# Optimization experiments

Measured on AMD Instinct MI355X. Metric: run time of the kernel, lower is better.

The kernel has to match this reference:

```python
import jax, jax.numpy as jnp
import numpy as np

V, D_IN = 32000, 300      # vocab, embedding dim (GRU input_size=300)
N, T = 4096, 64           # total nodes across batched graphs, tokens per node
B, NPG = 64, 64           # graphs, nodes per graph
E = 65536                 # total edges (avg degree 16)
RH, GH = 256, 256         # rnn_hidden_dim, gnn_hidden_dim


def gru_cell(x_proj, h, W_hh, b_hh):
    # x_proj = x @ W_ih.T + b_ih, shape [N, 3H]; PyTorch GRU gate order (r, z, n)
    gh = h @ W_hh.T + b_hh
    xr, xz, xn = jnp.split(x_proj, 3, axis=-1)
    hr, hz, hn = jnp.split(gh, 3, axis=-1)
    r = jax.nn.sigmoid(xr + hr)
    z = jax.nn.sigmoid(xz + hz)
    n = jnp.tanh(xn + r * hn)
    return (1.0 - z) * n + z * h


def setup_inputs() -> dict:
    key = jax.random.key(0)
    ks = jax.random.split(key, 16)
    tokens = jax.random.randint(ks[0], (N, T), 0, V)
    # edges live within a single graph (dgl.batch keeps graphs disjoint)
    edge_graph = jnp.arange(E) // (E // B)
    edge_src = edge_graph * NPG + jax.random.randint(ks[1], (E,), 0, NPG)
    edge_dst = edge_graph * NPG + jax.random.randint(ks[2], (E,), 0, NPG)
    graph_id = jnp.arange(N) // NPG
    local = jnp.arange(N) % NPG
    # node types: 0=history, 1=last_sentence (one per graph), 2=response (one per graph)
    node_type = jnp.where(local == NPG - 2, 1, jnp.where(local == NPG - 1, 2, 0))
    s = 0.02
    p = lambda k, shape: jax.random.normal(k, shape, dtype=jnp.float32) * s
    return dict(
        tokens=tokens, edge_src=edge_src, edge_dst=edge_dst,
        graph_id=graph_id, node_type=node_type,
        emb_table=p(ks[3], (V, D_IN)),
        W_ih_f=p(ks[4], (3 * RH, D_IN)), W_hh_f=p(ks[5], (3 * RH, RH)),
        b_ih_f=jnp.zeros((3 * RH,), jnp.float32), b_hh_f=jnp.zeros((3 * RH,), jnp.float32),
        W_ih_b=p(ks[6], (3 * RH, D_IN)), W_hh_b=p(ks[7], (3 * RH, RH)),
        b_ih_b=jnp.zeros((3 * RH,), jnp.float32), b_hh_b=jnp.zeros((3 * RH,), jnp.float32),
        W_g1=p(ks[8], (2 * RH, GH)), b_g1=jnp.zeros((GH,), jnp.float32),
        W_g2=p(ks[9], (GH, GH)), b_g2=jnp.zeros((GH,), jnp.float32),
        W_g3=p(ks[10], (GH, GH)), b_g3=jnp.zeros((GH,), jnp.float32),
        W_g4=p(ks[11], (GH, GH)), b_g4=jnp.zeros((GH,), jnp.float32),
    )


def reference(tokens, edge_src, edge_dst, graph_id, node_type, emb_table,
              W_ih_f, W_hh_f, b_ih_f, b_hh_f,
              W_ih_b, W_hh_b, b_ih_b, b_hh_b,
              W_g1, b_g1, W_g2, b_g2, W_g3, b_g3, W_g4, b_g4):
    x = emb_table[tokens]  # [N, T, 300]
    # Module keeps only output[:, -1, :]:
    #   forward half  = final forward hidden state (full scan over T)
    #   backward half = backward state after processing only timestep T-1
    #                   (i.e. one GRU cell step from zero state) -- exact math.
    xp_f = jnp.einsum('ntd,gd->ntg', x, W_ih_f) + b_ih_f  # [N, T, 3H]
    h0 = jnp.zeros((N, RH), x.dtype)

    def step(h, xp_t):
        return gru_cell(xp_t, h, W_hh_f, b_hh_f), None

    h_fwd, _ = jax.lax.scan(step, h0, jnp.swapaxes(xp_f, 0, 1))
    xp_b = x[:, -1] @ W_ih_b.T + b_ih_b
    h_bwd = gru_cell(xp_b, h0, W_hh_b, b_hh_b)
    h = jnp.concatenate([h_fwd, h_bwd], axis=-1)  # [N, 2H]

    # 4 GCN layers: sum-aggregate neighbor features (copy_src -> sum), then linear + ReLU
    for W, b in ((W_g1, b_g1), (W_g2, b_g2), (W_g3, b_g3), (W_g4, b_g4)):
        agg = jax.ops.segment_sum(h[edge_src], edge_dst, num_segments=N)
        h = jax.nn.relu(agg @ W + b)

    # per-graph readout by node type
    hist_m = (node_type == 0).astype(h.dtype)[:, None]
    last_m = (node_type == 1).astype(h.dtype)[:, None]
    resp_m = (node_type == 2).astype(h.dtype)[:, None]
    hist_sum = jax.ops.segment_sum(h * hist_m, graph_id, num_segments=B)
    hist_cnt = jax.ops.segment_sum(hist_m, graph_id, num_segments=B)
    batched_hist = hist_sum / hist_cnt
    batched_last = jax.ops.segment_sum(h * last_m, graph_id, num_segments=B)
    batched_resp = jax.ops.segment_sum(h * resp_m, graph_id, num_segments=B)
    return (batched_hist, batched_last, batched_resp)
```

## Files before the change

### kernel.cpp

```cpp
#include <hip/hip_runtime.h>
#include <cstddef>

#define NN_ 4096
#define TT_ 64
#define DIN 300
#define DINP 320
#define RH_ 256
#define G3_ 768
#define BB_ 64
#define EE_ 65536

typedef short bf16x8 __attribute__((ext_vector_type(8)));
typedef float f32x4 __attribute__((ext_vector_type(4)));
typedef unsigned short u16;

__device__ __forceinline__ u16 f2bf(float f) {
    unsigned u = __builtin_bit_cast(unsigned, f);
    u += 0x7fff + ((u >> 16) & 1);
    return (u16)(u >> 16);
}
__device__ __forceinline__ float bf2f(u16 v) {
    return __builtin_bit_cast(float, (unsigned)v << 16);
}

__device__ __forceinline__ void gload16(const void* g, void* l) {
    __builtin_amdgcn_global_load_lds(
        (const __attribute__((address_space(1))) unsigned*)g,
        (__attribute__((address_space(3))) unsigned*)l, 16, 0, 0);
}

#define MFMA16 __builtin_amdgcn_mfma_f32_16x16x32_bf16

__global__ void k_zero(float* __restrict__ p, long n) {
    for (long i = (long)blockIdx.x * blockDim.x + threadIdx.x; i < n;
         i += (long)gridDim.x * blockDim.x)
        p[i] = 0.f;
}

__global__ void k_cvt(const float* __restrict__ src, u16* __restrict__ dst,
                      int R, int C, int Cp) {
    long total = (long)R * Cp;
    for (long i = (long)blockIdx.x * blockDim.x + threadIdx.x; i < total;
         i += (long)gridDim.x * blockDim.x) {
        int r = (int)(i / Cp);
        int c = (int)(i - (long)r * Cp);
        dst[i] = (c < C) ? f2bf(src[(size_t)r * C + c]) : (u16)0;
    }
}

__global__ void k_cvtT(const float* __restrict__ W, u16* __restrict__ Wt, int K) {
    int total = 256 * K;
    for (int i = blockIdx.x * blockDim.x + threadIdx.x; i < total;
         i += gridDim.x * blockDim.x) {
        int c = i / K, k = i - c * K;
        Wt[i] = f2bf(W[(size_t)k * 256 + c]);
    }
}

__global__ void k_buildA(const int* __restrict__ src, const int* __restrict__ dst,
                         float* __restrict__ A) {
    int e = blockIdx.x * blockDim.x + threadIdx.x;
    if (e < EE_) {
        int g = src[e] >> 6, i = dst[e] & 63, j = src[e] & 63;
        atomicAdd(&A[(((g << 6) + i) << 6) + j], 1.f);
    }
}

__global__ __launch_bounds__(256) void k_trans(const float* __restrict__ h, int C,
                                               u16* __restrict__ hT) {
    __shared__ u16 Ls[64][72];
    int r0 = blockIdx.x * 64, c0 = blockIdx.y * 64;
    int tid = threadIdx.x;
    int r = tid >> 2, cq = tid & 3;
#pragma unroll
    for (int i = 0; i < 4; i++) {
        float4 v = *(const float4*)(h + (size_t)(r0 + r) * C + c0 + cq * 16 + i * 4);
        Ls[r][cq * 16 + i * 4 + 0] = f2bf(v.x);
        Ls[r][cq * 16 + i * 4 + 1] = f2bf(v.y);
        Ls[r][cq * 16 + i * 4 + 2] = f2bf(v.z);
        Ls[r][cq * 16 + i * 4 + 3] = f2bf(v.w);
    }
    __syncthreads();
    int c = tid >> 2, rq = tid & 3;
    u16 tmp[16];
#pragma unroll
    for (int i = 0; i < 16; i++) tmp[i] = Ls[rq * 16 + i][c];
    u16* o = hT + (size_t)(c0 + c) * NN_ + r0 + rq * 16;
    *(uint4*)o = ((const uint4*)tmp)[0];
    *(uint4*)(o + 8) = ((const uint4*)tmp)[1];
}

__global__ __launch_bounds__(256) void k_xproj(
    const u16* __restrict__ embbf, const u16* __restrict__ Wx,
    const float* __restrict__ bih, const float* __restrict__ bhh,
    u16* __restrict__ XP)
{
    __shared__ __align__(16) u16 As[2][64 * 32];
    __shared__ __align__(16) u16 Bs[2][64 * 32];
    const int tid = threadIdx.x;
    const int v0 = blockIdx.x * 64, c0 = blockIdx.y * 64;
    const int sr = tid >> 2, sq = tid & 3;
    const u16* pa = embbf + (size_t)(v0 + sr) * DINP + sq * 8;
    const u16* pb = Wx + (size_t)(c0 + sr) * DINP + sq * 8;

    const int lane = tid & 63, wave = tid >> 6;
    const int wr = wave >> 1, wc = wave & 1;
    const int l15 = lane & 15, l4 = lane >> 4;
    const int aoff = (wr * 32 + l15) * 32 + l4 * 8;
    const int boff = (wc * 32 + l15) * 32 + l4 * 8;
    f32x4 acc[2][2] = {};

    gload16(pa, &As[0][tid * 8]);
    gload16(pb, &Bs[0][tid * 8]);
    __syncthreads();
    constexpr int NSK = DINP / 32;
#pragma unroll
    for (int s = 0; s < NSK; s++) {
        if (s + 1 < NSK) {
            gload16(pa + (s + 1) * 32, &As[(s + 1) & 1][tid * 8]);
            gload16(pb + (s + 1) * 32, &Bs[(s + 1) & 1][tid * 8]);
        }
        const int b = s & 1;
        bf16x8 a0 = *(const bf16x8*)&As[b][aoff];
        bf16x8 a1 = *(const bf16x8*)&As[b][aoff + 512];
        bf16x8 b0 = *(const bf16x8*)&Bs[b][boff];
        bf16x8 b1 = *(const bf16x8*)&Bs[b][boff + 512];
        acc[0][0] = MFMA16(a0, b0, acc[0][0], 0, 0, 0);
        acc[0][1] = MFMA16(a0, b1, acc[0][1], 0, 0, 0);
        acc[1][0] = MFMA16(a1, b0, acc[1][0], 0, 0, 0);
        acc[1][1] = MFMA16(a1, b1, acc[1][1], 0, 0, 0);
        __syncthreads();
    }
#pragma unroll
    for (int fj = 0; fj < 2; fj++) {
        const int c = c0 + wc * 32 + fj * 16 + l15;
        const float bb = bih[c] + (c < 512 ? bhh[c] : 0.f);
#pragma unroll
        for (int fi = 0; fi < 2; fi++)
#pragma unroll
            for (int rg = 0; rg < 4; rg++) {
                const int v = v0 + wr * 32 + fi * 16 + l4 * 4 + rg;
                XP[(size_t)v * G3_ + c] = f2bf(acc[fi][fj][rg] + bb);
            }
    }
}

__global__ __launch_bounds__(512, 2) void k_scan(
    const int* __restrict__ tokens,
    const u16* __restrict__ XPROJ,
    const u16* __restrict__ Wh,
    const float* __restrict__ bhh,
    float* __restrict__ HA)
{
    __shared__ __align__(16) u16 hS[16 * RH_];
    __shared__ __align__(16) u16 XPs[3 * 16 * 256];
    __shared__ int toks[16 * 68];

    const int tid = threadIdx.x;
    const int n0 = blockIdx.x * 16;
    const int lane = tid & 63, wave = tid >> 6;
    const int l15 = lane & 15, l4 = lane >> 4;
    const int c0w = wave * 32;

    for (int idx = tid; idx < 16 * TT_; idx += 512) {
        int row = idx >> 6, tt = idx & 63;
        toks[row * 68 + tt] = tokens[(n0 + row) * TT_ + tt];
    }
    ((unsigned long long*)hS)[tid] = 0ull;
    ((unsigned long long*)hS)[512 + tid] = 0ull;

    bf16x8 Bv[3][2][8];
#pragma unroll
    for (int g = 0; g < 3; ++g)
#pragma unroll
        for (int f = 0; f < 2; ++f)
#pragma unroll
            for (int ks = 0; ks < 8; ++ks) {
                Bv[g][f][ks] = *(const bf16x8*)(
                    Wh + (size_t)(g * 256 + c0w + f * 16 + l15) * RH_ + ks * 32 + l4 * 8);
                asm volatile("" : "+v"(Bv[g][f][ks]));
            }

    const float bhn0 = bhh[512 + c0w + l15];
    const float bhn1 = bhh[512 + c0w + 16 + l15];

    const int srow = tid >> 5, sch = tid & 31;
    const int ssw = (((sch * 16) ^ ((srow >> 2) << 5)) >> 1);

    auto STAGE_XP = [&](int t) {
        int tok = toks[srow * 68 + t];
        const u16* src = XPROJ + (size_t)tok * G3_ + ssw;
#pragma unroll
        for (int g = 0; g < 3; ++g)
            gload16(src + g * 256, XPs + g * 4096 + tid * 8);
    };

    __syncthreads();

    STAGE_XP(0);

    f32x4 hprev[2] = {};

#pragma unroll 1
    for (int t = 0; t < TT_; ++t) {
        f32x4 acc[3][2];
#pragma unroll
        for (int g = 0; g < 3; ++g) { acc[g][0] = f32x4{}; acc[g][1] = f32x4{}; }
#pragma unroll
        for (int ks = 0; ks < 8; ++ks) {
            const int aa = (l15 * 512 + ks * 64 + l4 * 16) ^ ((l15 & 7) << 4);
            bf16x8 a = *(const bf16x8*)((const char*)hS + aa);
#pragma unroll
            for (int g = 0; g < 3; ++g) {
                acc[g][0] = MFMA16(a, Bv[g][0][ks], acc[g][0], 0, 0, 0);
                acc[g][1] = MFMA16(a, Bv[g][1][ks], acc[g][1], 0, 0, 0);
            }
        }
        __syncthreads();

#pragma unroll
        for (int f = 0; f < 2; ++f) {
            const int cc = c0w + f * 16 + l15;
            const float bhn = f == 0 ? bhn0 : bhn1;
#pragma unroll
            for (int rg = 0; rg < 4; ++rg) {
                const int r = l4 * 4 + rg;
                const int xb = r * 256 + ((((cc * 2) ^ ((r >> 2) << 5))) >> 1);
                float xr = bf2f(XPs[xb]);
                float xz = bf2f(XPs[4096 + xb]);
                float xn = bf2f(XPs[8192 + xb]);
                float gr = acc[0][f][rg];
                float gz = acc[1][f][rg];
                float gn = acc[2][f][rg];
                float hp = hprev[f][rg];
                float rr = 1.f / (1.f + __expf(-(xr + gr)));
                float zz = 1.f / (1.f + __expf(-(xz + gz)));
                float pre = xn + rr * (gn + bhn);
                float nv = 2.f / (1.f + __expf(-2.f * pre)) - 1.f;
                float hnew = (1.f - zz) * nv + zz * hp;
                hprev[f][rg] = hnew;
                if (t < TT_ - 1) {
                    const int ba = (r * 512 + cc * 2) ^ ((r & 7) << 4);
                    *(u16*)((char*)hS + ba) = f2bf(hnew);
                } else {
                    HA[(size_t)(n0 + r) * 512 + cc] = hnew;
                }
            }
        }
        __syncthreads();
        if (t < TT_ - 1) STAGE_XP(t + 1);
    }
}

template<bool XONLY>
__global__ __launch_bounds__(256) void k_step(
    const int* __restrict__ tokens, int t,
    const u16* __restrict__ embbf, const u16* __restrict__ Wx,
    const u16* __restrict__ Wh,
    const float* __restrict__ bih, const float* __restrict__ bhh,
    const u16* __restrict__ hbf_in, const float* __restrict__ hf_in,
    float* __restrict__ outf, int ostride, u16* __restrict__ outbf)
{
    constexpr int NSX = DINP / 32;
    constexpr int NS  = XONLY ? NSX : NSX + RH_ / 32;

    __shared__ __align__(16) u16 As[2][32 * 32];
    __shared__ __align__(16) u16 Bs[2][3 * 64 * 32];

    const int tid = threadIdx.x;
    const int n0 = blockIdx.x * 32;
    const int c0 = blockIdx.y * 64;

    const int sr = tid >> 2;
    const int sq = tid & 3;
    const int tok = (tid < 128) ? tokens[(n0 + sr) * TT_ + t] : 0;
    const u16* ax  = embbf + (size_t)tok * DINP + sq * 8;
    const u16* ah  = XONLY ? ax : hbf_in + (size_t)(n0 + sr) * RH_ + sq * 8;
    const u16* bx0 = Wx + (size_t)(0 * 256 + c0 + sr) * DINP + sq * 8;
    const u16* bx1 = Wx + (size_t)(1 * 256 + c0 + sr) * DINP + sq * 8;
    const u16* bx2 = Wx + (size_t)(2 * 256 + c0 + sr) * DINP + sq * 8;
    const u16* bh0 = XONLY ? ax : Wh + (size_t)(0 * 256 + c0 + sr) * RH_ + sq * 8;
    const u16* bh1 = XONLY ? ax : Wh + (size_t)(1 * 256 + c0 + sr) * RH_ + sq * 8;
    const u16* bh2 = XONLY ? ax : Wh + (size_t)(2 * 256 + c0 + sr) * RH_ + sq * 8;

    auto STAGE = [&](int b, int s) {
        u16* db = &Bs[b][tid * 8];
        if (s < NSX) {
            int kk = s * 32;
            if (tid < 128) gload16(ax + kk, &As[b][tid * 8]);
            gload16(bx0 + kk, db);
            gload16(bx1 + kk, db + 2048);
            gload16(bx2 + kk, db + 4096);
        } else {
            int kk = (s - NSX) * 32;
            if (tid < 128) gload16(ah + kk, &As[b][tid * 8]);
            gload16(bh0 + kk, db);
            gload16(bh1 + kk, db + 2048);
            gload16(bh2 + kk, db + 4096);
        }
    };

    const int lane = tid & 63;
    const int wave = tid >> 6;
    const int wr = wave >> 1, wc = wave & 1;
    const int l15 = lane & 15, l4 = lane >> 4;

    f32x4 aR[2] = {}, aZ[2] = {}, aXN[2] = {}, aHN[2] = {};

    const int aoff = (wr * 16 + l15) * 32 + l4 * 8;
    const int boff = (wc * 32 + l15) * 32 + l4 * 8;

    auto COMPUTE = [&](int b, bool xp) {
        bf16x8 a0 = *(const bf16x8*)&As[b][aoff];
        const u16* B = &Bs[b][0];
        bf16x8 r0 = *(const bf16x8*)&B[boff];
        bf16x8 r1 = *(const bf16x8*)&B[boff + 512];
        bf16x8 z0 = *(const bf16x8*)&B[2048 + boff];
        bf16x8 z1 = *(const bf16x8*)&B[2048 + boff + 512];
        bf16x8 n0f = *(const bf16x8*)&B[4096 + boff];
        bf16x8 n1f = *(const bf16x8*)&B[4096 + boff + 512];
        aR[0] = MFMA16(a0, r0, aR[0], 0, 0, 0);
        aR[1] = MFMA16(a0, r1, aR[1], 0, 0, 0);
        aZ[0] = MFMA16(a0, z0, aZ[0], 0, 0, 0);
        aZ[1] = MFMA16(a0, z1, aZ[1], 0, 0, 0);
        if (xp) {
            aXN[0] = MFMA16(a0, n0f, aXN[0], 0, 0, 0);
            aXN[1] = MFMA16(a0, n1f, aXN[1], 0, 0, 0);
        } else {
            aHN[0] = MFMA16(a0, n0f, aHN[0], 0, 0, 0);
            aHN[1] = MFMA16(a0, n1f, aHN[1], 0, 0, 0);
        }
    };

    STAGE(0, 0);
    __syncthreads();
#pragma unroll
    for (int s = 0; s < NS; ++s) {
        if (s + 1 < NS) STAGE((s + 1) & 1, s + 1);
        COMPUTE(s & 1, s < NSX);
        __syncthreads();
    }

#pragma unroll
    for (int fj = 0; fj < 2; ++fj) {
        const int c = c0 + wc * 32 + fj * 16 + l15;
        const float bR  = bih[c] + bhh[c];
        const float bZ  = bih[256 + c] + bhh[256 + c];
        const float bXN = bih[512 + c];
        const float bHN = bhh[512 + c];
#pragma unroll
        for (int rg = 0; rg < 4; ++rg) {
            const int n = n0 + wr * 16 + l4 * 4 + rg;
            float r  = 1.f / (1.f + __expf(-(aR[fj][rg] + bR)));
            float z  = 1.f / (1.f + __expf(-(aZ[fj][rg] + bZ)));
            float pre = aXN[fj][rg] + bXN + r * (aHN[fj][rg] + bHN);
            float nv = 2.f / (1.f + __expf(-2.f * pre)) - 1.f;
            float hp = XONLY ? 0.f : hf_in[(size_t)n * RH_ + c];
            float h  = (1.f - z) * nv + z * hp;
            outf[(size_t)n * ostride + c] = h;
            if (!XONLY) outbf[(size_t)n * RH_ + c] = f2bf(h);
        }
    }
}

__global__ __launch_bounds__(256) void k_agg(
    const u16* __restrict__ Abf, const u16* __restrict__ hT,
    u16* __restrict__ aggbf, int C)
{
    const int g = blockIdx.x, ct = blockIdx.y;
    const int lane = threadIdx.x & 63, wave = threadIdx.x >> 6;
    const int wi = wave >> 1, wcC = wave & 1;
    const int l15 = lane & 15, l4 = lane >> 4;
    f32x4 acc[2][2] = {};
#pragma unroll
    for (int kc = 0; kc < 2; kc++) {
        bf16x8 af[2], bf_[2];
#pragma unroll
        for (int fi = 0; fi < 2; fi++)
            af[fi] = *(const bf16x8*)(Abf + ((size_t)g * 64 + wi * 32 + fi * 16 + l15) * 64
                                      + kc * 32 + l4 * 8);
#pragma unroll
        for (int fj = 0; fj < 2; fj++)
            bf_[fj] = *(const bf16x8*)(hT + (size_t)(ct * 64 + wcC * 32 + fj * 16 + l15) * NN_
                                       + g * 64 + kc * 32 + l4 * 8);
#pragma unroll
        for (int fi = 0; fi < 2; fi++)
#pragma unroll
            for (int fj = 0; fj < 2; fj++)
                acc[fi][fj] = MFMA16(af[fi], bf_[fj], acc[fi][fj], 0, 0, 0);
    }
#pragma unroll
    for (int fi = 0; fi < 2; fi++)
#pragma unroll
        for (int fj = 0; fj < 2; fj++)
#pragma unroll
            for (int rg = 0; rg < 4; rg++) {
                int n = g * 64 + wi * 32 + fi * 16 + l4 * 4 + rg;
                int c = ct * 64 + wcC * 32 + fj * 16 + l15;
                aggbf[(size_t)n * C + c] = f2bf(acc[fi][fj][rg]);
            }
}

template<int K>
__global__ __launch_bounds__(256) void k_gcnM(
    const u16* __restrict__ Ag, const u16* __restrict__ Wt,
    const float* __restrict__ bias, float* __restrict__ outF)
{
    __shared__ __align__(16) u16 As[2][64 * 32];
    __shared__ __align__(16) u16 Bs[2][64 * 32];
    const int tid = threadIdx.x;
    const int n0 = blockIdx.x * 64, c0 = blockIdx.y * 64;
    const int sr = tid >> 2, sq = tid & 3;
    const u16* pa = Ag + (size_t)(n0 + sr) * K + sq * 8;
    const u16* pb = Wt + (size_t)(c0 + sr) * K + sq * 8;

    const int lane = tid & 63, wave = tid >> 6;
    const int wr = wave >> 1, wc = wave & 1;
    const int l15 = lane & 15, l4 = lane >> 4;
    const int aoff = (wr * 32 + l15) * 32 + l4 * 8;
    const int boff = (wc * 32 + l15) * 32 + l4 * 8;
    f32x4 acc[2][2] = {};

    gload16(pa, &As[0][tid * 8]);
    gload16(pb, &Bs[0][tid * 8]);
    __syncthreads();
    constexpr int NSK = K / 32;
#pragma unroll
    for (int s = 0; s < NSK; s++) {
        if (s + 1 < NSK) {
            gload16(pa + (s + 1) * 32, &As[(s + 1) & 1][tid * 8]);
            gload16(pb + (s + 1) * 32, &Bs[(s + 1) & 1][tid * 8]);
        }
        const int b = s & 1;
        bf16x8 a0 = *(const bf16x8*)&As[b][aoff];
        bf16x8 a1 = *(const bf16x8*)&As[b][aoff + 512];
        bf16x8 b0 = *(const bf16x8*)&Bs[b][boff];
        bf16x8 b1 = *(const bf16x8*)&Bs[b][boff + 512];
        acc[0][0] = MFMA16(a0, b0, acc[0][0], 0, 0, 0);
        acc[0][1] = MFMA16(a0, b1, acc[0][1], 0, 0, 0);
        acc[1][0] = MFMA16(a1, b0, acc[1][0], 0, 0, 0);
        acc[1][1] = MFMA16(a1, b1, acc[1][1], 0, 0, 0);
        __syncthreads();
    }
#pragma unroll
    for (int fj = 0; fj < 2; fj++) {
        const int c = c0 + wc * 32 + fj * 16 + l15;
        const float bb = bias[c];
#pragma unroll
        for (int fi = 0; fi < 2; fi++)
#pragma unroll
            for (int rg = 0; rg < 4; rg++) {
                const int n = n0 + wr * 32 + fi * 16 + l4 * 4 + rg;
                outF[(size_t)n * 256 + c] = fmaxf(acc[fi][fj][rg] + bb, 0.f);
            }
    }
}

__global__ void k_readout(const float* __restrict__ h, const int* __restrict__ gid,
                          const int* __restrict__ ntype, float* __restrict__ out,
                          float* __restrict__ cnt)
{
    for (int idx = blockIdx.x * blockDim.x + threadIdx.x; idx < NN_ * 256;
         idx += gridDim.x * blockDim.x) {
        int n = idx >> 8, c = idx & 255;
        float v = h[idx];
        int g = gid[n], t = ntype[n];
        if (t == 0) {
            atomicAdd(&out[g * 256 + c], v);
            if (c == 0) atomicAdd(&cnt[g], 1.f);
        } else if (t == 1) {
            atomicAdd(&out[16384 + g * 256 + c], v);
        } else {
            atomicAdd(&out[32768 + g * 256 + c], v);
        }
    }
}

__global__ void k_finalize(float* __restrict__ out, const float* __restrict__ cnt)
{
    int idx = blockIdx.x * blockDim.x + threadIdx.x;
    out[idx] /= cnt[idx >> 8];
}

extern "C" void kernel_launch(void* const* d_in, const int* in_sizes, int n_in,
                              void* d_out, int out_size, void* d_ws, size_t ws_size,
                              hipStream_t stream)
{
    const int*   tokens = (const int*)d_in[0];
    const int*   esrc   = (const int*)d_in[1];
    const int*   edst   = (const int*)d_in[2];
    const int*   gid    = (const int*)d_in[3];
    const int*   ntype  = (const int*)d_in[4];
    const float* emb    = (const float*)d_in[5];
    const float* W_ih_f = (const float*)d_in[6];
    const float* W_hh_f = (const float*)d_in[7];
    const float* b_ih_f = (const float*)d_in[8];
    const float* b_hh_f = (const float*)d_in[9];
    const float* W_ih_b = (const float*)d_in[10];
    const float* b_ih_b = (const float*)d_in[12];
    const float* b_hh_b = (const float*)d_in[13];
    const float* Wg[4]  = {(const float*)d_in[14], (const float*)d_in[16],
                           (const float*)d_in[18], (const float*)d_in[20]};
    const float* bg[4]  = {(const float*)d_in[15], (const float*)d_in[17],
                           (const float*)d_in[19], (const float*)d_in[21]};
    float* out = (float*)d_out;

    float* hF    = (float*)d_ws;
    float* Af    = hF;
    u16*   embbf = (u16*)(hF + (size_t)NN_ * RH_);
    u16*   wxf   = embbf + 32000L * DINP;
    u16*   whf   = wxf + (size_t)G3_ * DINP;
    u16*   wxb   = whf + (size_t)G3_ * RH_;
    u16*   wtg   = wxb + (size_t)G3_ * DINP;
    u16*   Abf   = wtg + 256L * 512;
    u16*   XPROJ = Abf + 64L * 64 * 64;
    u16*   hT    = XPROJ;
    u16*   aggb  = hT + 512L * NN_;
    float* HA    = (float*)(XPROJ + 32000L * G3_);
    float* CNT   = HA + (size_t)NN_ * 512;

    k_cvt<<<2048, 256, 0, stream>>>(emb, embbf, 32000, DIN, DINP);
    k_cvt<<<256, 256, 0, stream>>>(W_ih_f, wxf, G3_, DIN, DINP);
    k_cvt<<<256, 256, 0, stream>>>(W_hh_f, whf, G3_, RH_, RH_);
    k_cvt<<<256, 256, 0, stream>>>(W_ih_b, wxb, G3_, DIN, DINP);
    k_zero<<<256, 256, 0, stream>>>(Af, 64L * 64 * 64);
    k_buildA<<<256, 256, 0, stream>>>(esrc, edst, Af);
    k_cvt<<<256, 256, 0, stream>>>(Af, Abf, 64 * 64, 64, 64);

    k_xproj<<<dim3(500, 12), 256, 0, stream>>>(embbf, wxf, b_ih_f, b_hh_f, XPROJ);
    k_scan<<<256, 512, 0, stream>>>(tokens, XPROJ, whf, b_hh_f, HA);

    k_step<true><<<dim3(128, 4), 256, 0, stream>>>(
        tokens, TT_ - 1, embbf, wxb, nullptr, b_ih_b, b_hh_b,
        nullptr, nullptr, HA + 256, 512, nullptr);

    k_trans<<<dim3(64, 8), 256, 0, stream>>>(HA, 512, hT);
    for (int l = 0; l < 4; l++) {
        int K = (l == 0) ? 512 : 256;
        k_cvtT<<<128, 256, 0, stream>>>(Wg[l], wtg, K);
        k_agg<<<dim3(64, K / 64), 256, 0, stream>>>(Abf, hT, aggb, K);
        if (K == 512)
            k_gcnM<512><<<dim3(64, 4), 256, 0, stream>>>(aggb, wtg, bg[l], hF);
        else
            k_gcnM<256><<<dim3(64, 4), 256, 0, stream>>>(aggb, wtg, bg[l], hF);
        if (l < 3) k_trans<<<dim3(64, 4), 256, 0, stream>>>(hF, 256, hT);
    }

    k_zero<<<256, 256, 0, stream>>>(out, 49152);
    k_zero<<<1, 64, 0, stream>>>(CNT, 64);
    k_readout<<<2048, 256, 0, stream>>>(hF, gid, ntype, out, CNT);
    k_finalize<<<64, 256, 0, stream>>>(out, CNT);
}
```

Before: 449.6 us.

## Split GRU scan across 16 waves and double-buffer gate-input staging

The recurrent scan kernel now launches 1024 threads per block, so each of 16 waves owns 16 hidden columns instead of 32. This halves the per-wave MFMA chain and the register-resident weights on the serial critical path. The x-projection staging buffer is double-buffered and prefetched two steps ahead, so global loads overlap more with compute. The costs are larger shared memory use and more waves contending at the two barriers per timestep.

```diff
diff --git a/kernel.cpp b/kernel.cpp
--- a/kernel.cpp
+++ b/kernel.cpp
@@ -145,7 +145,7 @@
     }
 }
 
-__global__ __launch_bounds__(512, 2) void k_scan(
+__global__ __launch_bounds__(1024, 4) void k_scan(
     const int* __restrict__ tokens,
     const u16* __restrict__ XPROJ,
     const u16* __restrict__ Wh,
@@ -153,102 +153,92 @@
     float* __restrict__ HA)
 {
     __shared__ __align__(16) u16 hS[16 * RH_];
-    __shared__ __align__(16) u16 XPs[3 * 16 * 256];
+    __shared__ __align__(16) u16 XPs[2][3 * 16 * 256];
     __shared__ int toks[16 * 68];
 
     const int tid = threadIdx.x;
     const int n0 = blockIdx.x * 16;
     const int lane = tid & 63, wave = tid >> 6;
     const int l15 = lane & 15, l4 = lane >> 4;
-    const int c0w = wave * 32;
-
-    for (int idx = tid; idx < 16 * TT_; idx += 512) {
-        int row = idx >> 6, tt = idx & 63;
+    const int c0w = wave * 16;
+
+    {
+        int row = tid >> 6, tt = tid & 63;
         toks[row * 68 + tt] = tokens[(n0 + row) * TT_ + tt];
     }
     ((unsigned long long*)hS)[tid] = 0ull;
-    ((unsigned long long*)hS)[512 + tid] = 0ull;
-
-    bf16x8 Bv[3][2][8];
+
+    bf16x8 Bv[3][8];
 #pragma unroll
     for (int g = 0; g < 3; ++g)
 #pragma unroll
-        for (int f = 0; f < 2; ++f)
-#pragma unroll
-            for (int ks = 0; ks < 8; ++ks) {
-                Bv[g][f][ks] = *(const bf16x8*)(
-                    Wh + (size_t)(g * 256 + c0w + f * 16 + l15) * RH_ + ks * 32 + l4 * 8);
-                asm volatile("" : "+v"(Bv[g][f][ks]));
-            }
-
-    const float bhn0 = bhh[512 + c0w + l15];
-    const float bhn1 = bhh[512 + c0w + 16 + l15];
-
-    const int srow = tid >> 5, sch = tid & 31;
-    const int ssw = (((sch * 16) ^ ((srow >> 2) << 5)) >> 1);
-
-    auto STAGE_XP = [&](int t) {
-        int tok = toks[srow * 68 + t];
-        const u16* src = XPROJ + (size_t)tok * G3_ + ssw;
-#pragma unroll
-        for (int g = 0; g < 3; ++g)
-            gload16(src + g * 256, XPs + g * 4096 + tid * 8);
+        for (int ks = 0; ks < 8; ++ks)
+            Bv[g][ks] = *(const bf16x8*)(
+                Wh + (size_t)(g * 256 + c0w + l15) * RH_ + ks * 32 + l4 * 8);
+
+    const float bhn = bhh[512 + c0w + l15];
+
+    __syncthreads();
+
+    auto STAGE_XP = [&](int t, int b) {
+        {
+            int c = tid;
+            int g = c >> 9, cw = c & 511, row = cw >> 5, sch = cw & 31;
+            int tok = toks[row * 68 + t];
+            int ssw = ((sch * 16) ^ ((row >> 2) << 5)) >> 1;
+            gload16(XPROJ + (size_t)tok * G3_ + g * 256 + ssw, &XPs[b][c * 8]);
+        }
+        if (tid < 512) {
+            int c = 1024 + tid;
+            int g = c >> 9, cw = c & 511, row = cw >> 5, sch = cw & 31;
+            int tok = toks[row * 68 + t];
+            int ssw = ((sch * 16) ^ ((row >> 2) << 5)) >> 1;
+            gload16(XPROJ + (size_t)tok * G3_ + g * 256 + ssw, &XPs[b][c * 8]);
+        }
     };
 
-    __syncthreads();
-
-    STAGE_XP(0);
-
-    f32x4 hprev[2] = {};
+    STAGE_XP(0, 0);
+    STAGE_XP(1, 1);
+
+    f32x4 hprev = {};
 
 #pragma unroll 1
     for (int t = 0; t < TT_; ++t) {
-        f32x4 acc[3][2];
-#pragma unroll
-        for (int g = 0; g < 3; ++g) { acc[g][0] = f32x4{}; acc[g][1] = f32x4{}; }
+        f32x4 acc[3] = {};
 #pragma unroll
         for (int ks = 0; ks < 8; ++ks) {
             const int aa = (l15 * 512 + ks * 64 + l4 * 16) ^ ((l15 & 7) << 4);
             bf16x8 a = *(const bf16x8*)((const char*)hS + aa);
-#pragma unroll
-            for (int g = 0; g < 3; ++g) {
-                acc[g][0] = MFMA16(a, Bv[g][0][ks], acc[g][0], 0, 0, 0);
-                acc[g][1] = MFMA16(a, Bv[g][1][ks], acc[g][1], 0, 0, 0);
+            acc[0] = MFMA16(a, Bv[0][ks], acc[0], 0, 0, 0);
+            acc[1] = MFMA16(a, Bv[1][ks], acc[1], 0, 0, 0);
+            acc[2] = MFMA16(a, Bv[2][ks], acc[2], 0, 0, 0);
+        }
+        __syncthreads();
+
+        const u16* XB = XPs[t & 1];
+        const int cc = c0w + l15;
+#pragma unroll
+        for (int rg = 0; rg < 4; ++rg) {
+            const int r = l4 * 4 + rg;
+            const int xb = r * 256 + ((((cc * 2) ^ ((r >> 2) << 5))) >> 1);
+            float xr = bf2f(XB[xb]);
+            float xz = bf2f(XB[4096 + xb]);
+            float xn = bf2f(XB[8192 + xb]);
+            float rr = 1.f / (1.f + __expf(-(xr + acc[0][rg])));
+            float zz = 1.f / (1.f + __expf(-(xz + acc[1][rg])));
+            float pre = xn + rr * (acc[2][rg] + bhn);
+            float nv = 2.f / (1.f + __expf(-2.f * pre)) - 1.f;
+            float hnew = nv + zz * (hprev[rg] - nv);
+            hprev[rg] = hnew;
+            if (t < TT_ - 1) {
+                const int ba = (r * 512 + cc * 2) ^ ((r & 7) << 4);
+                *(u16*)((char*)hS + ba) = f2bf(hnew);
+            } else {
+                HA[(size_t)(n0 + r) * 512 + cc] = hnew;
             }
         }
         __syncthreads();
-
-#pragma unroll
-        for (int f = 0; f < 2; ++f) {
-            const int cc = c0w + f * 16 + l15;
-            const float bhn = f == 0 ? bhn0 : bhn1;
-#pragma unroll
-            for (int rg = 0; rg < 4; ++rg) {
-                const int r = l4 * 4 + rg;
-                const int xb = r * 256 + ((((cc * 2) ^ ((r >> 2) << 5))) >> 1);
-                float xr = bf2f(XPs[xb]);
-                float xz = bf2f(XPs[4096 + xb]);
-                float xn = bf2f(XPs[8192 + xb]);
-                float gr = acc[0][f][rg];
-                float gz = acc[1][f][rg];
-                float gn = acc[2][f][rg];
-                float hp = hprev[f][rg];
-                float rr = 1.f / (1.f + __expf(-(xr + gr)));
-                float zz = 1.f / (1.f + __expf(-(xz + gz)));
-                float pre = xn + rr * (gn + bhn);
-                float nv = 2.f / (1.f + __expf(-2.f * pre)) - 1.f;
-                float hnew = (1.f - zz) * nv + zz * hp;
-                hprev[f][rg] = hnew;
-                if (t < TT_ - 1) {
-                    const int ba = (r * 512 + cc * 2) ^ ((r & 7) << 4);
-                    *(u16*)((char*)hS + ba) = f2bf(hnew);
-                } else {
-                    HA[(size_t)(n0 + r) * 512 + cc] = hnew;
-                }
-            }
-        }
-        __syncthreads();
-        if (t < TT_ - 1) STAGE_XP(t + 1);
+        if (t + 2 < TT_) STAGE_XP(t + 2, t & 1);
     }
 }
 
@@ -528,7 +518,7 @@
     k_cvt<<<256, 256, 0, stream>>>(Af, Abf, 64 * 64, 64, 64);
 
     k_xproj<<<dim3(500, 12), 256, 0, stream>>>(embbf, wxf, b_ih_f, b_hh_f, XPROJ);
-    k_scan<<<256, 512, 0, stream>>>(tokens, XPROJ, whf, b_hh_f, HA);
+    k_scan<<<256, 1024, 0, stream>>>(tokens, XPROJ, whf, b_hh_f, HA);
 
     k_step<true><<<dim3(128, 4), 256, 0, stream>>>(
         tokens, TT_ - 1, embbf, wxb, nullptr, b_ih_b, b_hh_b,
```

Measured after the change: 516.9 us. +15.0%, slower.
